# Optimization experiments

Measured on AMD Instinct MI355X. Metric: run time of the kernel, lower is better.

## Reference

```python
import jax, jax.numpy as jnp
import numpy as np

B, C, T = 2, 2, 4
N_SRC = 49152   # npix at level 6 (12 * 4^6)
N_TGT = 12288   # npix at level 5 (12 * 4^5)
D = 128


def setup_inputs() -> dict:
    key = jax.random.key(0)
    k1, k2, k3, k4 = jax.random.split(key, 4)
    x = jax.random.normal(k1, (B, C, T, N_SRC, D), dtype=jnp.float32)
    parent_map = jax.random.randint(k2, (N_SRC,), 0, N_TGT)
    W = jax.random.normal(k3, (D, D), dtype=jnp.float32) * 0.05  # Conv1d kernel_size=1 weight [out,in]
    b = jax.random.normal(k4, (D,), dtype=jnp.float32) * 0.05    # Conv1d bias
    return {"x": x, "parent_map": parent_map, "W": W, "b": b}


def reference(x, parent_map, W, b):
    # HEALPix downsample: scatter-add mean pooling over parent_map, then 1x1 conv.
    Bs, Cs, Ts, N, Dd = x.shape
    # flatten (b c t) and put pixel axis first for segment_sum: [N, BCT, D]
    x2 = x.reshape(Bs * Cs * Ts, N, Dd).transpose(1, 0, 2)
    sums = jax.ops.segment_sum(x2, parent_map, num_segments=N_TGT)          # [N_TGT, BCT, D]
    cnt = jax.ops.segment_sum(jnp.ones((N,), x.dtype), parent_map, num_segments=N_TGT)
    mean = sums / jnp.clip(cnt, 1e-6)[:, None, None]
    # 1x1 Conv1d over channel dim D: y = W @ mean + b
    out = jnp.einsum('mbd,ed->mbe', mean, W) + b                            # [N_TGT, BCT, D]
    return out.transpose(1, 0, 2).reshape(Bs, Cs, Ts, N_TGT, Dd)
```

## Files before the change

### kernel.cpp

```cpp
#include <hip/hip_runtime.h>
#include <stdint.h>

#define NSRC 49152
#define NTGT 12288
#define DIM  128
#define MPER 4
#define ROWS (MPER*16)
#define CAP  32
#define OSTR 132

using short8  = __attribute__((ext_vector_type(8))) short;
using short4v = __attribute__((ext_vector_type(4))) short;
using bf16x8  = __attribute__((ext_vector_type(8))) __bf16;
using f32x4   = __attribute__((ext_vector_type(4))) float;

__device__ __forceinline__ short f2bf(float f){
  unsigned int u = __float_as_uint(f);
  return (short)((u + 0x7fffu + ((u >> 16) & 1u)) >> 16);
}

__global__ void k_setup(const int* __restrict__ pm,
                        int* __restrict__ counts, int* __restrict__ child,
                        const float* __restrict__ W, short* __restrict__ Wt){
  const int b = blockIdx.x;
  if (b < 192){
    int i = b * 256 + threadIdx.x;
    int p = pm[i];
    int pos = atomicAdd(&counts[p], 1);
    if (pos < CAP) child[p * CAP + pos] = i;
  } else {
    int t  = (b - 192) * 256 + threadIdx.x;
    int e  = t & 127;
    int kk = t >> 7;
    const float4* src = (const float4*)(W + (size_t)e * DIM + kk * 8);
    float4 u = src[0], v = src[1];
    short8 h;
    h[0]=f2bf(u.x); h[1]=f2bf(u.y); h[2]=f2bf(u.z); h[3]=f2bf(u.w);
    h[4]=f2bf(v.x); h[5]=f2bf(v.y); h[6]=f2bf(v.z); h[7]=f2bf(v.w);
    *reinterpret_cast<short8*>(Wt + ((size_t)kk * 128 + e) * 8) = h;
  }
}

__global__ __launch_bounds__(256, 4) void k_fused(
    const float* __restrict__ x, const short* __restrict__ Wt,
    const float* __restrict__ bias,
    const int* __restrict__ counts, const int* __restrict__ child,
    float* __restrict__ out)
{
  __shared__ __align__(16) char smem[ROWS * OSTR * 4];
  short* s_mean = (short*)smem;
  float* s_out  = (float*)smem;
  const int tid = threadIdx.x;
  const int m0  = blockIdx.x * MPER;

  {
    const int o  = tid & 7;
    const int rr = tid >> 3;
    #pragma unroll
    for (int it = 0; it < 2; ++it){
      const int r   = it * 32 + rr;
      const int m   = m0 + (r >> 4);
      const int bct = r & 15;
      int cnt = counts[m]; cnt = (cnt > CAP) ? CAP : cnt;
      const int* cl = child + (size_t)m * CAP;
      const int4 i03 = *reinterpret_cast<const int4*>(cl);
      const int4 i47 = *reinterpret_cast<const int4*>(cl + 4);
      const float* rowb = x + (size_t)bct * NSRC * DIM;
      f32x4 acc[4];
      #pragma unroll
      for (int s = 0; s < 4; ++s) acc[s] = (f32x4){0.f, 0.f, 0.f, 0.f};

      auto G2 = [&](int n0, int n1){
        const f32x4* p0 = (const f32x4*)(rowb + (size_t)n0 * DIM) + o;
        const f32x4* p1 = (const f32x4*)(rowb + (size_t)n1 * DIM) + o;
        f32x4 v0[4], v1[4];
        #pragma unroll
        for (int s = 0; s < 4; ++s) v0[s] = __builtin_nontemporal_load(p0 + s * 8);
        #pragma unroll
        for (int s = 0; s < 4; ++s) v1[s] = __builtin_nontemporal_load(p1 + s * 8);
        #pragma unroll
        for (int s = 0; s < 4; ++s) acc[s] += v0[s] + v1[s];
      };
      auto G1 = [&](int n0){
        const f32x4* p0 = (const f32x4*)(rowb + (size_t)n0 * DIM) + o;
        #pragma unroll
        for (int s = 0; s < 4; ++s) acc[s] += __builtin_nontemporal_load(p0 + s * 8);
      };

      if (cnt > 1) G2(i03.x, i03.y);
      if (cnt > 3) G2(i03.z, i03.w);
      if (cnt > 5) G2(i47.x, i47.y);
      if (cnt > 7) G2(i47.z, i47.w);
      int c = (cnt < 8) ? (cnt & ~1) : 8;
      for (; c < cnt; ++c) G1(cl[c]);

      const float inv = (cnt > 0) ? (1.0f / (float)cnt) : 0.0f;
      const int rsw = (r & 7) << 3;
      #pragma unroll
      for (int s = 0; s < 4; ++s){
        const int col = s * 32 + o * 4;
        short4v h;
        h[0] = f2bf(acc[s][0] * inv); h[1] = f2bf(acc[s][1] * inv);
        h[2] = f2bf(acc[s][2] * inv); h[3] = f2bf(acc[s][3] * inv);
        *reinterpret_cast<short4v*>(&s_mean[r * DIM + (col ^ rsw)]) = h;
      }
    }
  }

  __syncthreads();

  const int w  = tid >> 6;
  const int l  = tid & 63;
  const int lr = l & 15;
  const int kg = l >> 4;
  f32x4 acc[8];
  #pragma unroll
  for (int n = 0; n < 8; ++n) acc[n] = (f32x4){0.f, 0.f, 0.f, 0.f};

  #pragma unroll 1
  for (int ks = 0; ks < 4; ++ks){
    const int k = ks * 32 + kg * 8;
    const int row = w * 16 + lr;
    bf16x8 af = *reinterpret_cast<bf16x8*>(&s_mean[row * DIM + (k ^ ((row & 7) << 3))]);
    const short* wp = Wt + ((size_t)(ks * 4 + kg) * 128 + lr) * 8;
    #pragma unroll
    for (int n = 0; n < 8; ++n){
      bf16x8 bfr = *reinterpret_cast<const bf16x8*>(wp + n * 128);
      acc[n] = __builtin_amdgcn_mfma_f32_16x16x32_bf16(af, bfr, acc[n], 0, 0, 0);
    }
  }

  float bv[8];
  #pragma unroll
  for (int n = 0; n < 8; ++n) bv[n] = bias[n * 16 + lr];

  __syncthreads();
  #pragma unroll
  for (int j = 0; j < 4; ++j){
    const int grl = w * 16 + (l >> 4) * 4 + j;
    #pragma unroll
    for (int n = 0; n < 8; ++n)
      s_out[grl * OSTR + n * 16 + lr] = acc[n][j] + bv[n];
  }
  __syncthreads();
  #pragma unroll
  for (int r2 = 0; r2 < 4; ++r2){
    const int bct = w * 4 + r2;
    #pragma unroll
    for (int it2 = 0; it2 < 2; ++it2){
      const int f  = it2 * 64 + l;
      const int mi = f >> 5, d4 = f & 31;
      f32x4 v = *reinterpret_cast<f32x4*>(&s_out[(mi * 16 + bct) * OSTR + d4 * 4]);
      float* gp = out + ((size_t)bct * NTGT + m0 + mi) * DIM + d4 * 4;
      __builtin_nontemporal_store(v, reinterpret_cast<f32x4*>(gp));
    }
  }
}

extern "C" void kernel_launch(void* const* d_in, const int* in_sizes, int n_in,
                              void* d_out, int out_size, void* d_ws, size_t ws_size,
                              hipStream_t stream) {
  const float* x    = (const float*)d_in[0];
  const int*   pm   = (const int*)  d_in[1];
  const float* W    = (const float*)d_in[2];
  const float* bias = (const float*)d_in[3];
  float* out = (float*)d_out;

  int*   counts = (int*)d_ws;
  int*   child  = counts + NTGT;
  short* Wt     = (short*)(child + NTGT * CAP);

  hipMemsetAsync(counts, 0, NTGT * sizeof(int), stream);
  k_setup<<<200, 256, 0, stream>>>(pm, counts, child, W, Wt);
  k_fused<<<NTGT/MPER, 256, 0, stream>>>(x, Wt, bias, counts, child, out);
}
```

Before: 115.5 us.

## Merge memset, setup and fused kernels into one persistent cooperative kernel

Replaces the memset plus two kernel launches with a single cooperative persistent kernel. It zeroes the counts, converts W, builds the child lists, and then loops over output tiles, with grid.sync barriers between the phases. This removes launch gaps and per-launch overhead. In exchange it adds two grid-wide barriers, and because the grid is capped by occupancy, each block now processes several tiles serially.

New measurement: 277.9 us. 2.41x slower.

```diff
diff --git a/kernel.cpp b/kernel.cpp
--- a/kernel.cpp
+++ b/kernel.cpp
@@ -1,10 +1,14 @@
 #include <hip/hip_runtime.h>
+#include <hip/hip_cooperative_groups.h>
 #include <stdint.h>
+
+namespace cg = cooperative_groups;
 
 #define NSRC 49152
 #define NTGT 12288
 #define DIM  128
 #define MPER 4
+#define NTILE (NTGT/MPER)
 #define ROWS (MPER*16)
 #define CAP  32
 #define OSTR 132
@@ -19,17 +23,22 @@
   return (short)((u + 0x7fffu + ((u >> 16) & 1u)) >> 16);
 }
 
-__global__ void k_setup(const int* __restrict__ pm,
-                        int* __restrict__ counts, int* __restrict__ child,
-                        const float* __restrict__ W, short* __restrict__ Wt){
-  const int b = blockIdx.x;
-  if (b < 192){
-    int i = b * 256 + threadIdx.x;
-    int p = pm[i];
-    int pos = atomicAdd(&counts[p], 1);
-    if (pos < CAP) child[p * CAP + pos] = i;
-  } else {
-    int t  = (b - 192) * 256 + threadIdx.x;
+__global__ __launch_bounds__(256, 4) void k_all(
+    const float* __restrict__ x, const int* __restrict__ pm,
+    const float* __restrict__ W, const float* __restrict__ bias,
+    int* __restrict__ counts, int* __restrict__ child,
+    short* __restrict__ Wt, float* __restrict__ out)
+{
+  __shared__ __align__(16) char smem[ROWS * OSTR * 4];
+  short* s_mean = (short*)smem;
+  float* s_out  = (float*)smem;
+  const int tid  = threadIdx.x;
+  const int gid  = blockIdx.x * 256 + tid;
+  const int gtot = gridDim.x * 256;
+  cg::grid_group grid = cg::this_grid();
+
+  for (int i = gid; i < NTGT; i += gtot) counts[i] = 0;
+  for (int t = gid; t < 2048; t += gtot){
     int e  = t & 127;
     int kk = t >> 7;
     const float4* src = (const float4*)(W + (size_t)e * DIM + kk * 8);
@@ -39,120 +48,122 @@
     h[4]=f2bf(v.x); h[5]=f2bf(v.y); h[6]=f2bf(v.z); h[7]=f2bf(v.w);
     *reinterpret_cast<short8*>(Wt + ((size_t)kk * 128 + e) * 8) = h;
   }
-}
+  __threadfence();
+  grid.sync();
 
-__global__ __launch_bounds__(256, 4) void k_fused(
-    const float* __restrict__ x, const short* __restrict__ Wt,
-    const float* __restrict__ bias,
-    const int* __restrict__ counts, const int* __restrict__ child,
-    float* __restrict__ out)
-{
-  __shared__ __align__(16) char smem[ROWS * OSTR * 4];
-  short* s_mean = (short*)smem;
-  float* s_out  = (float*)smem;
-  const int tid = threadIdx.x;
-  const int m0  = blockIdx.x * MPER;
+  for (int i = gid; i < NSRC; i += gtot){
+    int p = pm[i];
+    int pos = atomicAdd(&counts[p], 1);
+    if (pos < CAP) child[p * CAP + pos] = i;
+  }
+  __threadfence();
+  grid.sync();
 
-  {
-    const int o  = tid & 7;
-    const int rr = tid >> 3;
-    #pragma unroll
-    for (int it = 0; it < 2; ++it){
-      const int r   = it * 32 + rr;
-      const int m   = m0 + (r >> 4);
-      const int bct = r & 15;
-      int cnt = counts[m]; cnt = (cnt > CAP) ? CAP : cnt;
-      const int* cl = child + (size_t)m * CAP;
-      const int4 i03 = *reinterpret_cast<const int4*>(cl);
-      const int4 i47 = *reinterpret_cast<const int4*>(cl + 4);
-      const float* rowb = x + (size_t)bct * NSRC * DIM;
-      f32x4 acc[4];
+  for (int tile = blockIdx.x; tile < NTILE; tile += gridDim.x){
+    const int m0 = tile * MPER;
+    __syncthreads();
+
+    {
+      const int o  = tid & 7;
+      const int rr = tid >> 3;
       #pragma unroll
-      for (int s = 0; s < 4; ++s) acc[s] = (f32x4){0.f, 0.f, 0.f, 0.f};
+      for (int it = 0; it < 2; ++it){
+        const int r   = it * 32 + rr;
+        const int m   = m0 + (r >> 4);
+        const int bct = r & 15;
+        int cnt = counts[m]; cnt = (cnt > CAP) ? CAP : cnt;
+        const int* cl = child + (size_t)m * CAP;
+        const int4 i03 = *reinterpret_cast<const int4*>(cl);
+        const int4 i47 = *reinterpret_cast<const int4*>(cl + 4);
+        const float* rowb = x + (size_t)bct * NSRC * DIM;
+        f32x4 acc[4];
+        #pragma unroll
+        for (int s = 0; s < 4; ++s) acc[s] = (f32x4){0.f, 0.f, 0.f, 0.f};
 
-      auto G2 = [&](int n0, int n1){
-        const f32x4* p0 = (const f32x4*)(rowb + (size_t)n0 * DIM) + o;
-        const f32x4* p1 = (const f32x4*)(rowb + (size_t)n1 * DIM) + o;
-        f32x4 v0[4], v1[4];
+        auto G2 = [&](int n0, int n1){
+          const f32x4* p0 = (const f32x4*)(rowb + (size_t)n0 * DIM) + o;
+          const f32x4* p1 = (const f32x4*)(rowb + (size_t)n1 * DIM) + o;
+          f32x4 v0[4], v1[4];
+          #pragma unroll
+          for (int s = 0; s < 4; ++s) v0[s] = __builtin_nontemporal_load(p0 + s * 8);
+          #pragma unroll
+          for (int s = 0; s < 4; ++s) v1[s] = __builtin_nontemporal_load(p1 + s * 8);
+          #pragma unroll
+          for (int s = 0; s < 4; ++s) acc[s] += v0[s] + v1[s];
+        };
+        auto G1 = [&](int n0){
+          const f32x4* p0 = (const f32x4*)(rowb + (size_t)n0 * DIM) + o;
+          #pragma unroll
+          for (int s = 0; s < 4; ++s) acc[s] += __builtin_nontemporal_load(p0 + s * 8);
+        };
+
+        if (cnt > 1) G2(i03.x, i03.y);
+        if (cnt > 3) G2(i03.z, i03.w);
+        if (cnt > 5) G2(i47.x, i47.y);
+        if (cnt > 7) G2(i47.z, i47.w);
+        int c = (cnt < 8) ? (cnt & ~1) : 8;
+        for (; c < cnt; ++c) G1(cl[c]);
+
+        const float inv = (cnt > 0) ? (1.0f / (float)cnt) : 0.0f;
+        const int rsw = (r & 7) << 3;
         #pragma unroll
-        for (int s = 0; s < 4; ++s) v0[s] = __builtin_nontemporal_load(p0 + s * 8);
-        #pragma unroll
-        for (int s = 0; s < 4; ++s) v1[s] = __builtin_nontemporal_load(p1 + s * 8);
-        #pragma unroll
-        for (int s = 0; s < 4; ++s) acc[s] += v0[s] + v1[s];
-      };
-      auto G1 = [&](int n0){
-        const f32x4* p0 = (const f32x4*)(rowb + (size_t)n0 * DIM) + o;
-        #pragma unroll
-        for (int s = 0; s < 4; ++s) acc[s] += __builtin_nontemporal_load(p0 + s * 8);
-      };
-
-      if (cnt > 1) G2(i03.x, i03.y);
-      if (cnt > 3) G2(i03.z, i03.w);
-      if (cnt > 5) G2(i47.x, i47.y);
-      if (cnt > 7) G2(i47.z, i47.w);
-      int c = (cnt < 8) ? (cnt & ~1) : 8;
-      for (; c < cnt; ++c) G1(cl[c]);
-
-      const float inv = (cnt > 0) ? (1.0f / (float)cnt) : 0.0f;
-      const int rsw = (r & 7) << 3;
-      #pragma unroll
-      for (int s = 0; s < 4; ++s){
-        const int col = s * 32 + o * 4;
-        short4v h;
-        h[0] = f2bf(acc[s][0] * inv); h[1] = f2bf(acc[s][1] * inv);
-        h[2] = f2bf(acc[s][2] * inv); h[3] = f2bf(acc[s][3] * inv);
-        *reinterpret_cast<short4v*>(&s_mean[r * DIM + (col ^ rsw)]) = h;
+        for (int s = 0; s < 4; ++s){
+          const int col = s * 32 + o * 4;
+          short4v h;
+          h[0] = f2bf(acc[s][0] * inv); h[1] = f2bf(acc[s][1] * inv);
+          h[2] = f2bf(acc[s][2] * inv); h[3] = f2bf(acc[s][3] * inv);
+          *reinterpret_cast<short4v*>(&s_mean[r * DIM + (col ^ rsw)]) = h;
+        }
       }
     }
-  }
 
-  __syncthreads();
+    __syncthreads();
 
-  const int w  = tid >> 6;
-  const int l  = tid & 63;
-  const int lr = l & 15;
-  const int kg = l >> 4;
-  f32x4 acc[8];
-  #pragma unroll
-  for (int n = 0; n < 8; ++n) acc[n] = (f32x4){0.f, 0.f, 0.f, 0.f};
+    const int w  = tid >> 6;
+    const int l  = tid & 63;
+    const int lr = l & 15;
+    const int kg = l >> 4;
+    f32x4 acc[8];
+    #pragma unroll
+    for (int n = 0; n < 8; ++n) acc[n] = (f32x4){0.f, 0.f, 0.f, 0.f};
 
-  #pragma unroll 1
-  for (int ks = 0; ks < 4; ++ks){
-    const int k = ks * 32 + kg * 8;
-    const int row = w * 16 + lr;
-    bf16x8 af = *reinterpret_cast<bf16x8*>(&s_mean[row * DIM + (k ^ ((row & 7) << 3))]);
-    const short* wp = Wt + ((size_t)(ks * 4 + kg) * 128 + lr) * 8;
+    #pragma unroll 1
+    for (int ks = 0; ks < 4; ++ks){
+      const int k = ks * 32 + kg * 8;
+      const int row = w * 16 + lr;
+      bf16x8 af = *reinterpret_cast<bf16x8*>(&s_mean[row * DIM + (k ^ ((row & 7) << 3))]);
+      const short* wp = Wt + ((size_t)(ks * 4 + kg) * 128 + lr) * 8;
+      #pragma unroll
+      for (int n = 0; n < 8; ++n){
+        bf16x8 bfr = *reinterpret_cast<const bf16x8*>(wp + n * 128);
+        acc[n] = __builtin_amdgcn_mfma_f32_16x16x32_bf16(af, bfr, acc[n], 0, 0, 0);
+      }
+    }
+
+    float bv[8];
     #pragma unroll
-    for (int n = 0; n < 8; ++n){
-      bf16x8 bfr = *reinterpret_cast<const bf16x8*>(wp + n * 128);
-      acc[n] = __builtin_amdgcn_mfma_f32_16x16x32_bf16(af, bfr, acc[n], 0, 0, 0);
+    for (int n = 0; n < 8; ++n) bv[n] = bias[n * 16 + lr];
+
+    __syncthreads();
+    #pragma unroll
+    for (int j = 0; j < 4; ++j){
+      const int grl = w * 16 + (l >> 4) * 4 + j;
+      #pragma unroll
+      for (int n = 0; n < 8; ++n)
+        s_out[grl * OSTR + n * 16 + lr] = acc[n][j] + bv[n];
     }
-  }
-
-  float bv[8];
-  #pragma unroll
-  for (int n = 0; n < 8; ++n) bv[n] = bias[n * 16 + lr];
-
-  __syncthreads();
-  #pragma unroll
-  for (int j = 0; j < 4; ++j){
-    const int grl = w * 16 + (l >> 4) * 4 + j;
+    __syncthreads();
     #pragma unroll
-    for (int n = 0; n < 8; ++n)
-      s_out[grl * OSTR + n * 16 + lr] = acc[n][j] + bv[n];
-  }
-  __syncthreads();
-  #pragma unroll
-  for (int r2 = 0; r2 < 4; ++r2){
-    const int bct = w * 4 + r2;
-    #pragma unroll
-    for (int it2 = 0; it2 < 2; ++it2){
-      const int f  = it2 * 64 + l;
-      const int mi = f >> 5, d4 = f & 31;
-      f32x4 v = *reinterpret_cast<f32x4*>(&s_out[(mi * 16 + bct) * OSTR + d4 * 4]);
-      float* gp = out + ((size_t)bct * NTGT + m0 + mi) * DIM + d4 * 4;
-      __builtin_nontemporal_store(v, reinterpret_cast<f32x4*>(gp));
+    for (int r2 = 0; r2 < 4; ++r2){
+      const int bct = w * 4 + r2;
+      #pragma unroll
+      for (int it2 = 0; it2 < 2; ++it2){
+        const int f  = it2 * 64 + l;
+        const int mi = f >> 5, d4 = f & 31;
+        f32x4 v = *reinterpret_cast<f32x4*>(&s_out[(mi * 16 + bct) * OSTR + d4 * 4]);
+        float* gp = out + ((size_t)bct * NTGT + m0 + mi) * DIM + d4 * 4;
+        __builtin_nontemporal_store(v, reinterpret_cast<f32x4*>(gp));
+      }
     }
   }
 }
@@ -170,7 +181,14 @@
   int*   child  = counts + NTGT;
   short* Wt     = (short*)(child + NTGT * CAP);
 
-  hipMemsetAsync(counts, 0, NTGT * sizeof(int), stream);
-  k_setup<<<200, 256, 0, stream>>>(pm, counts, child, W, Wt);
-  k_fused<<<NTGT/MPER, 256, 0, stream>>>(x, Wt, bias, counts, child, out);
+  int nb = 0;
+  (void)hipOccupancyMaxActiveBlocksPerMultiprocessor(&nb, k_all, 256, 0);
+  if (nb < 1) nb = 1;
+  int grid = nb * 256;
+  if (grid > 1024) grid = 1024;
+
+  void* args[] = {(void*)&x, (void*)&pm, (void*)&W, (void*)&bias,
+                  (void*)&counts, (void*)&child, (void*)&Wt, (void*)&out};
+  (void)hipLaunchCooperativeKernel((const void*)k_all, dim3(grid), dim3(256),
+                                   args, 0, stream);
 }
```
